# Performance work log

Hardware: AMD Instinct MI355X
Metric: run time of the kernel (lower is better)

Reference implementation:

```python
import jax, jax.numpy as jnp
import numpy as np

N_NODES = 50000
N_EDGES = 500000
IN_DIM = 32
HID = 64
NUM_GRAPHS = 64


def _inv(d):
    # 1/d with inf -> 0, as in PyG HypergraphConv
    return jnp.where(d > 0, 1.0 / d, 0.0)


def hypergraph_conv(xh, row0, row1, W, b, n_hnodes, n_hedges):
    """PyG HypergraphConv (heads=1, no attention, unit hyperedge weights).
    xh: (n_hnodes, din) hyper-node features; row0: hyper-node ids, row1: hyperedge ids.
    Index n_hnodes / n_hedges is a padding slot for masked-out incidences.
    """
    xw = xh @ W                                   # (n_hnodes, dout) Theta
    xw = jnp.concatenate([xw, jnp.zeros((1, xw.shape[1]), xw.dtype)], axis=0)
    ones = jnp.ones(row0.shape[0], xw.dtype)
    D = _inv(jax.ops.segment_sum(ones, row0, num_segments=n_hnodes + 1))  # node degree^-1
    B = _inv(jax.ops.segment_sum(ones, row1, num_segments=n_hedges + 1))  # edge size^-1
    # node -> hyperedge aggregation, scaled by B
    he = jax.ops.segment_sum(xw[row0], row1, num_segments=n_hedges + 1) * B[:, None]
    # hyperedge -> node aggregation, scaled by D
    out = jax.ops.segment_sum(he[row1], row0, num_segments=n_hnodes + 1) * D[:, None]
    return out[:n_hnodes] + b


def setup_inputs() -> dict:
    key = jax.random.key(0)
    ks = jax.random.split(key, 12)
    x = jax.random.normal(ks[0], (N_NODES, 16), jnp.float32)
    edge_attr = jax.random.normal(ks[1], (N_EDGES, IN_DIM), jnp.float32)
    edge_index = jax.random.randint(ks[2], (2, N_EDGES), 0, N_NODES, dtype=jnp.int64)
    batch = jnp.sort(jax.random.randint(ks[3], (N_NODES,), 0, NUM_GRAPHS, dtype=jnp.int64))
    node_imp = jax.random.uniform(ks[4], (N_NODES,), jnp.float32)
    s = 0.05
    W0 = jax.random.normal(ks[5], (IN_DIM, HID), jnp.float32) * s
    b0 = jax.random.normal(ks[6], (HID,), jnp.float32) * s
    W1 = jax.random.normal(ks[7], (HID, HID), jnp.float32) * s
    b1 = jax.random.normal(ks[8], (HID,), jnp.float32) * s
    W2 = jax.random.normal(ks[9], (HID, HID), jnp.float32) * s
    b2 = jax.random.normal(ks[10], (HID,), jnp.float32) * s
    return {"x": x, "edge_attr": edge_attr, "edge_index": edge_index, "batch": batch,
            "node_imp": node_imp, "W0": W0, "b0": b0, "W1": W1, "b1": b1,
            "W2": W2, "b2": b2, "num_graphs": NUM_GRAPHS}


def reference(x, edge_attr, edge_index, batch, node_imp, W0, b0, W1, b1, W2, b2, num_graphs):
    N = x.shape[0]
    E = edge_index.shape[1]
    edge_imp = jnp.minimum(node_imp[edge_index[0]], node_imp[edge_index[1]])
    # --- Dual Hypergraph Transform (get_DHT) ---
    row0 = jnp.repeat(jnp.arange(E), 2)            # hyper-node = original edge id
    row1 = edge_index.T.reshape(-1)                # hyperedge  = original node id
    deg = jax.ops.segment_sum(jnp.ones(2 * E, jnp.float32), row1, num_segments=N)
    keep = deg[row1] != 1.0                        # drop incidences of degree-1 hyperedges
    row0 = jnp.where(keep, row0, E)                # redirect dropped entries to padding slot
    row1 = jnp.where(keep, row1, N + E)
    # self-loops: hyperedge ids N..N+E-1 (equivalent to torch's max_edge+1.., since
    # unused hyperedge slots receive nothing and B^-1 there is 0)
    row0 = jnp.concatenate([row0, jnp.arange(E)])
    row1 = jnp.concatenate([row1, N + jnp.arange(E)])
    edge_batch = batch[edge_index[0]]              # == hyperedge_index[1].reshape(-1,2)[:,0]
    # --- conv stack (dropout in eval mode = identity) ---
    h = edge_attr * edge_imp[:, None]
    xs = []
    for (W, b) in ((W0, b0), (W1, b1), (W2, b2)):
        h = jax.nn.relu(hypergraph_conv(h, row0, row1, W, b, E, N + E))
        h = h * edge_imp[:, None]
        xs.append(h)
    gh = jnp.concatenate(
        [jax.ops.segment_sum(h_i, edge_batch, num_segments=num_graphs) for h_i in xs], axis=1)
    return gh
```

## Files before the change

### kernel.cpp

```cpp
#include <hip/hip_runtime.h>
#include <hip/hip_bf16.h>
#include <cstdint>
#include <cstddef>

typedef unsigned short u16;
typedef unsigned int   u32;
typedef short bf16x8 __attribute__((ext_vector_type(8)));
typedef float f32x4  __attribute__((ext_vector_type(4)));

struct __align__(16) ERec {
  u32 uv;
  float rc, iurc, ivrc;
  float ie; u32 bat; u32 pad0, pad1;
};

__device__ __forceinline__ float bf2f(u16 v){ return __uint_as_float(((u32)v)<<16); }
__device__ __forceinline__ u16 f2bf(float f){
  u32 x = __float_as_uint(f);
  return (u16)((x + 0x7FFFu + ((x>>16)&1u)) >> 16);
}
__device__ __forceinline__ void atomAddF(float* p, float v){ unsafeAtomicAdd(p, v); }
__device__ __forceinline__ float rlanef(float v, int q){
  return __int_as_float(__builtin_amdgcn_readlane(__float_as_int(v), q));
}

__global__ void kzero(int* p, int n){
  int i = blockIdx.x*blockDim.x + threadIdx.x;
  if(i < n) p[i] = 0;
}

__global__ void kdeg2(const int* __restrict__ ei0, const int* __restrict__ ei1,
                      int* __restrict__ deg0, int* __restrict__ deg1, int E){
  int e = blockIdx.x*blockDim.x + threadIdx.x;
  if(e >= E) return;
  atomicAdd(&deg0[ei0[e]], 1);
  atomicAdd(&deg1[ei1[e]], 1);
}

__global__ __launch_bounds__(256) void ktilesum(const int* __restrict__ deg0,
                                                const int* __restrict__ deg1,
                                                int* __restrict__ tsum,
                                                int N, int nt){
  __shared__ int sh[256];
  const int b = blockIdx.x;
  const int* deg = (b < nt) ? deg0 : deg1;
  const int tile = (b < nt) ? b : b - nt;
  const int t = threadIdx.x;
  const int i = tile*256 + t;
  sh[t] = (i < N) ? deg[i] : 0;
  __syncthreads();
  for(int s = 128; s > 0; s >>= 1){
    if(t < s) sh[t] += sh[t+s];
    __syncthreads();
  }
  if(t == 0) tsum[b] = sh[0];
}
__global__ __launch_bounds__(256) void kmid(int* __restrict__ tsum,
                                            int* __restrict__ off0,
                                            int* __restrict__ off1,
                                            int N, int nt){
  __shared__ int sh[256];
  const int b = blockIdx.x;
  int* ts = tsum + b*nt;
  const int t = threadIdx.x;
  sh[t] = (t < nt) ? ts[t] : 0;
  __syncthreads();
  for(int s = 1; s < 256; s <<= 1){
    int x = (t >= s) ? sh[t-s] : 0;
    __syncthreads();
    sh[t] += x;
    __syncthreads();
  }
  if(t < nt) ts[t] = (t == 0) ? 0 : sh[t-1];
  if(t == 255){ int* off = b ? off1 : off0; off[N] = sh[255]; }
}
__global__ __launch_bounds__(256) void kapply(const int* __restrict__ deg0,
                                              const int* __restrict__ deg1,
                                              const int* __restrict__ tsum,
                                              int* __restrict__ off0,
                                              int* __restrict__ off1,
                                              float* __restrict__ dinv,
                                              int N, int nt){
  __shared__ int sh[256];
  const int b = blockIdx.x;
  const int* deg = (b < nt) ? deg0 : deg1;
  int*       off = (b < nt) ? off0 : off1;
  const int tile = (b < nt) ? b : b - nt;
  const int base = tsum[b];
  const int t = threadIdx.x;
  const int i = tile*256 + t;
  sh[t] = (i < N) ? deg[i] : 0;
  __syncthreads();
  for(int s = 1; s < 256; s <<= 1){
    int x = (t >= s) ? sh[t-s] : 0;
    __syncthreads();
    sh[t] += x;
    __syncthreads();
  }
  if(i < N){
    off[i] = base + ((t == 0) ? 0 : sh[t-1]);
    if(b < nt){
      int d = deg0[i] + deg1[i];
      dinv[i] = (d > 1) ? (1.f/(float)d) : 0.f;
    }
  }
}

__global__ void kperm(const int* __restrict__ ei0, const int* __restrict__ ei1,
                      const float* __restrict__ nimp, const float* __restrict__ dinv,
                      const int* __restrict__ batch, const int* __restrict__ off0,
                      int* __restrict__ cur0, ERec* __restrict__ rec,
                      int* __restrict__ iperm, float* __restrict__ impO, int E){
  int e = blockIdx.x*blockDim.x + threadIdx.x;
  if(e >= E) return;
  int u = ei0[e], v = ei1[e];
  int pos = off0[u] + atomicAdd(&cur0[u], 1);
  float iu = dinv[u], iv = dinv[v];
  float rc = (iu > 0.f && iv > 0.f) ? (1.f/3.f)
           : ((iu > 0.f || iv > 0.f) ? 0.5f : 1.f);
  float ie = fminf(nimp[u], nimp[v]);
  ERec r;
  r.uv = (u32)u | ((u32)v << 16);
  r.rc = rc; r.iurc = iu*rc; r.ivrc = iv*rc;
  r.ie = ie; r.bat = (u32)batch[u]; r.pad0 = 0; r.pad1 = 0;
  rec[pos]  = r;
  iperm[e]  = pos;
  impO[e]   = ie;
}

__global__ void kfillv(const int* __restrict__ ei1, const int* __restrict__ iperm,
                       const int* __restrict__ off1, int* __restrict__ cur1,
                       int* __restrict__ list1, int E){
  int e = blockIdx.x*blockDim.x + threadIdx.x;
  if(e >= E) return;
  int v = ei1[e];
  list1[off1[v] + atomicAdd(&cur1[v], 1)] = iperm[e];
}

__global__ void kprepw(const float* __restrict__ W0, u16* __restrict__ wf0,
                       const float* __restrict__ W1, u16* __restrict__ wf1,
                       const float* __restrict__ W2, u16* __restrict__ wf2){
  const int b = blockIdx.x;
  const float* W; u16* wf; int NC, sbase;
  if(b == 0){ W = W0; wf = wf0; NC = 1; sbase = 0; }
  else if(b <= 2){ W = W1; wf = wf1; NC = 2; sbase = (b-1)*256; }
  else { W = W2; wf = wf2; NC = 2; sbase = (b-3)*256; }
  int s = sbase + threadIdx.x;
  if(s >= 4*NC*64) return;
  int lane = s & 63;
  int c    = (s >> 6) % NC;
  int tt   = s / (NC*64);
  int n  = tt*16 + (lane & 15);
  int k0 = c*32 + (lane >> 4)*8;
  #pragma unroll
  for(int j = 0; j < 8; j++)
    wf[(size_t)s*8 + j] = f2bf(W[(size_t)(k0 + j)*64 + n]);
}

__global__ __launch_bounds__(256) void kgemm0(const float* __restrict__ srcf,
                                              u16* __restrict__ buf,
                                              const u16* __restrict__ wf,
                                              const float* __restrict__ impO,
                                              const int* __restrict__ iperm,
                                              int E){
  const int t    = threadIdx.x;
  const int wv   = t >> 6;
  const int lane = t & 63;
  const int quad = lane >> 4;
  const int l15  = lane & 15;
  const int row0 = blockIdx.x*64 + wv*16;
  if(row0 >= E) return;

  bf16x8 bfr[4];
  #pragma unroll
  for(int i = 0; i < 4; i++)
    bfr[i] = *(const bf16x8*)(wf + ((size_t)i*64 + lane)*8);

  const int myrow = row0 + l15;
  const float* s = srcf + (size_t)myrow*32 + quad*8;
  const float sc = impO[myrow];
  const int ip = iperm[myrow];
  f32x4 v0 = *(const f32x4*)s;
  f32x4 v1 = *(const f32x4*)(s+4);
  bf16x8 afr;
  afr[0]=(short)f2bf(v0.x*sc); afr[1]=(short)f2bf(v0.y*sc);
  afr[2]=(short)f2bf(v0.z*sc); afr[3]=(short)f2bf(v0.w*sc);
  afr[4]=(short)f2bf(v1.x*sc); afr[5]=(short)f2bf(v1.y*sc);
  afr[6]=(short)f2bf(v1.z*sc); afr[7]=(short)f2bf(v1.w*sc);

  int dr[4];
  #pragma unroll
  for(int r = 0; r < 4; r++) dr[r] = __shfl(ip, quad*4 + r);

  #pragma unroll
  for(int tt = 0; tt < 4; tt++){
    f32x4 a = {0.f,0.f,0.f,0.f};
    a = __builtin_amdgcn_mfma_f32_16x16x32_bf16(afr, bfr[tt], a, 0, 0, 0);
    const int n = tt*16 + l15;
    #pragma unroll
    for(int r = 0; r < 4; r++)
      buf[(size_t)dr[r]*64 + n] = f2bf(a[r]);
  }
}

__global__ __launch_bounds__(256) void kagg(const u16* __restrict__ buf,
                                            const int* __restrict__ off0,
                                            const int* __restrict__ off1,
                                            const int* __restrict__ list1,
                                            u16* __restrict__ heb, int N){
  const int t = threadIdx.x, wv = t >> 6, lane = t & 63;
  const int n = blockIdx.x*4 + wv;
  if(n >= N) return;
  const int rsub = lane >> 3, cb = lane & 7;
  float acc[8];
  #pragma unroll
  for(int k = 0; k < 8; k++) acc[k] = 0.f;

  auto accum = [&](uint4 x){
    acc[0] += bf2f((u16)x.x); acc[1] += bf2f((u16)(x.x>>16));
    acc[2] += bf2f((u16)x.y); acc[3] += bf2f((u16)(x.y>>16));
    acc[4] += bf2f((u16)x.z); acc[5] += bf2f((u16)(x.z>>16));
    acc[6] += bf2f((u16)x.w); acc[7] += bf2f((u16)(x.w>>16));
  };
  const uint4 zero4 = {0,0,0,0};

  {
    const int s0 = off0[n], d0 = off0[n+1] - s0;
    const u16* base = buf + (size_t)s0*64;
    int j = 0;
    for(; j + 8 <= d0; j += 8)
      accum(*(const uint4*)(base + (size_t)(j+rsub)*64 + cb*8));
    if(j < d0)
      accum((rsub < d0-j) ? *(const uint4*)(base + (size_t)(j+rsub)*64 + cb*8) : zero4);
  }
  {
    const int s1 = off1[n], d1 = off1[n+1] - s1;
    int j = 0;
    for(; j + 8 <= d1; j += 8){
      int e = list1[s1 + j + rsub];
      accum(*(const uint4*)(buf + (size_t)e*64 + cb*8));
    }
    if(j < d1){
      uint4 x = zero4;
      if(rsub < d1-j){
        int e = list1[s1 + j + rsub];
        x = *(const uint4*)(buf + (size_t)e*64 + cb*8);
      }
      accum(x);
    }
  }
  #pragma unroll
  for(int m = 8; m <= 32; m <<= 1)
    #pragma unroll
    for(int k = 0; k < 8; k++) acc[k] += __shfl_xor(acc[k], m);
  if(rsub == 0){
    u32 o[4];
    #pragma unroll
    for(int k = 0; k < 4; k++)
      o[k] = (u32)f2bf(acc[2*k]) | ((u32)f2bf(acc[2*k+1]) << 16);
    *(uint4*)(heb + (size_t)n*64 + cb*8) = make_uint4(o[0],o[1],o[2],o[3]);
  }
}

template<bool DO_GEMM>
__global__ __launch_bounds__(256, 3) void kfused(u16* __restrict__ buf,
                                                 const u16* __restrict__ heb,
                                                 const f32x4* __restrict__ rec4,
                                                 const float* __restrict__ bias,
                                                 const u16* __restrict__ wf,
                                                 float* __restrict__ ghL,
                                                 int E){
  constexpr int HTSZ = DO_GEMM ? 4*16*72 : 4;
  __shared__ __align__(16) u16 hT[HTSZ];
  const int t = threadIdx.x, wv = t >> 6, lane = t & 63;
  const int quad = lane >> 4, l15 = lane & 15;
  const float bd = bias[lane];

  bf16x8 bfr[8];
  if(DO_GEMM){
    #pragma unroll
    for(int i = 0; i < 8; i++)
      bfr[i] = *(const bf16x8*)(wf + ((size_t)i*64 + lane)*8);
  }

  float pool = 0.f;
  int cur_g = -1;
  const int base = __builtin_amdgcn_readfirstlane((int)(blockIdx.x*256) + wv*64);
  u16* hTw = DO_GEMM ? &hT[wv*1152] : &hT[0];

  u32 uvp = 0; f32x4 cf = {0.f,0.f,0.f,0.f}; int bt = 0;
  if(base < E){
    f32x4 w0 = rec4[(size_t)(base+l15)*2];
    f32x4 w1 = rec4[(size_t)(base+l15)*2 + 1];
    uvp = __float_as_uint(w0.x);
    cf.x = w0.y; cf.y = w0.z; cf.z = w0.w; cf.w = w1.x;
    bt  = __float_as_int(w1.y);
  }

  #pragma unroll
  for(int it = 0; it < 4; it++){
    const int r0 = base + it*16;
    if(r0 < E){
      u16 bv[16], hu[16], hv[16];
      const u16* bufr = buf + (size_t)r0*64;
      #pragma unroll
      for(int q = 0; q < 16; q++){
        const u32 uv = (u32)__builtin_amdgcn_readlane((int)uvp, q);
        hv[q] = heb[(size_t)(uv >> 16)*64 + lane];
        hu[q] = heb[(size_t)(uv & 0xffffu)*64 + lane];
        bv[q] = bufr[q*64 + lane];
      }
      u32 uvpN = uvp; f32x4 cfN = cf; int btN = bt;
      if(it < 3){
        const int r1 = r0 + 16;
        if(r1 < E){
          f32x4 w0 = rec4[(size_t)(r1+l15)*2];
          f32x4 w1 = rec4[(size_t)(r1+l15)*2 + 1];
          uvpN = __float_as_uint(w0.x);
          cfN.x = w0.y; cfN.y = w0.z; cfN.z = w0.w; cfN.w = w1.x;
          btN  = __float_as_int(w1.y);
        }
      }
      const int bFirst = __builtin_amdgcn_readlane(bt, 0);
      const int bLast  = __builtin_amdgcn_readlane(bt, 15);
      if(bFirst != cur_g){
        if(cur_g >= 0) atomAddF(&ghL[cur_g*192 + lane], pool);
        pool = 0.f; cur_g = bFirst;
      }
      if(bFirst == bLast){
        #pragma unroll
        for(int q = 0; q < 16; q++){
          const float rc   = rlanef(cf.x, q);
          const float iurc = rlanef(cf.y, q);
          const float ivrc = rlanef(cf.z, q);
          const float ie   = rlanef(cf.w, q);
          float o = fmaxf(fmaf(bf2f(bv[q]), rc,
                          fmaf(bf2f(hu[q]), iurc,
                          fmaf(bf2f(hv[q]), ivrc, bd))), 0.f) * ie;
          pool += o;
          if(DO_GEMM) hTw[q*72 + lane] = f2bf(o);
        }
      } else {
        #pragma unroll
        for(int q = 0; q < 16; q++){
          const float rc   = rlanef(cf.x, q);
          const float iurc = rlanef(cf.y, q);
          const float ivrc = rlanef(cf.z, q);
          const float ie   = rlanef(cf.w, q);
          const int   bq   = __builtin_amdgcn_readlane(bt, q);
          float o = fmaxf(fmaf(bf2f(bv[q]), rc,
                          fmaf(bf2f(hu[q]), iurc,
                          fmaf(bf2f(hv[q]), ivrc, bd))), 0.f) * ie;
          if(bq != cur_g){
            if(cur_g >= 0) atomAddF(&ghL[cur_g*192 + lane], pool);
            pool = 0.f; cur_g = bq;
          }
          pool += o;
          if(DO_GEMM) hTw[q*72 + lane] = f2bf(o);
        }
      }
      if(DO_GEMM){
        bf16x8 afr0 = *(const bf16x8*)&hTw[l15*72 + quad*8];
        bf16x8 afr1 = *(const bf16x8*)&hTw[l15*72 + 32 + quad*8];
        #pragma unroll
        for(int tt = 0; tt < 4; tt++){
          f32x4 a = {0.f,0.f,0.f,0.f};
          a = __builtin_amdgcn_mfma_f32_16x16x32_bf16(afr0, bfr[tt*2+0], a, 0, 0, 0);
          a = __builtin_amdgcn_mfma_f32_16x16x32_bf16(afr1, bfr[tt*2+1], a, 0, 0, 0);
          const int n = tt*16 + l15;
          #pragma unroll
          for(int r = 0; r < 4; r++)
            buf[(size_t)(r0 + quad*4 + r)*64 + n] = f2bf(a[r]);
        }
      }
      uvp = uvpN; cf = cfN; bt = btN;
    }
  }
  if(cur_g >= 0) atomAddF(&ghL[cur_g*192 + lane], pool);
}

__global__ void kfinal(const float* __restrict__ gh, float* __restrict__ out, int n){
  int i = blockIdx.x*blockDim.x + threadIdx.x;
  if(i < n) out[i] = gh[i];
}

extern "C" void kernel_launch(void* const* d_in, const int* in_sizes, int n_in,
                              void* d_out, int out_size, void* d_ws, size_t ws_size,
                              hipStream_t stream) {
  const float* edge_attr = (const float*)d_in[1];
  const int*   ei        = (const int*)d_in[2];
  const int*   batch     = (const int*)d_in[3];
  const float* nimp      = (const float*)d_in[4];
  const float* Ws[3] = { (const float*)d_in[5], (const float*)d_in[7], (const float*)d_in[9] };
  const float* bs[3] = { (const float*)d_in[6], (const float*)d_in[8], (const float*)d_in[10] };

  const int E = in_sizes[1] / 32;
  const int N = in_sizes[4];
  const int* ei0 = ei;
  const int* ei1 = ei + E;

  char* p = (char*)d_ws;
  auto carve = [&](size_t bytes)->char*{
    char* r = p; p += (bytes + 255) & ~(size_t)255; return r;
  };
  const int nt = (N + 255)/256;
  int*   deg0  = (int*)  carve((size_t)4*N*4);
  int*   deg1  = deg0 + N;
  int*   cur0  = deg0 + 2*N;
  int*   cur1  = deg0 + 3*N;
  float* dinv  = (float*)carve((size_t)N*4);
  int*   off0  = (int*)  carve((size_t)(N+1)*4);
  int*   off1  = (int*)  carve((size_t)(N+1)*4);
  int*   tsum  = (int*)  carve((size_t)2*nt*4);
  int*   iperm = (int*)  carve((size_t)E*4);
  float* impO  = (float*)carve((size_t)E*4);
  int*   list1 = (int*)  carve((size_t)E*4);
  ERec*  rec   = (ERec*) carve((size_t)E*sizeof(ERec));
  u16*   heb   = (u16*)  carve((size_t)N*64*2);
  u16*   buf   = (u16*)  carve((size_t)E*64*2);
  float* gh    = (float*)carve((size_t)64*192*4);
  u16*   wfs[3];
  for(int l = 0; l < 3; l++) wfs[l] = (u16*)carve((size_t)4096*2);

  kzero<<<(4*N+255)/256, 256, 0, stream>>>(deg0, 4*N);
  kzero<<<(12288+255)/256, 256, 0, stream>>>((int*)gh, 12288);
  kdeg2<<<(E+255)/256, 256, 0, stream>>>(ei0, ei1, deg0, deg1, E);
  ktilesum<<<2*nt, 256, 0, stream>>>(deg0, deg1, tsum, N, nt);
  kmid<<<2, 256, 0, stream>>>(tsum, off0, off1, N, nt);
  kapply<<<2*nt, 256, 0, stream>>>(deg0, deg1, tsum, off0, off1, dinv, N, nt);
  kperm<<<(E+255)/256, 256, 0, stream>>>(ei0, ei1, nimp, dinv, batch, off0, cur0,
                                         rec, iperm, impO, E);
  kfillv<<<(E+255)/256, 256, 0, stream>>>(ei1, iperm, off1, cur1, list1, E);
  kprepw<<<5, 256, 0, stream>>>(Ws[0], wfs[0], Ws[1], wfs[1], Ws[2], wfs[2]);

  const int nbG = (E + 63)/64;
  const int nbA = (N + 3)/4;
  const int nbF = (E + 255)/256;

  kgemm0<<<nbG, 256, 0, stream>>>(edge_attr, buf, wfs[0], impO, iperm, E);
  kagg<<<nbA, 256, 0, stream>>>(buf, off0, off1, list1, heb, N);
  kfused<true ><<<nbF, 256, 0, stream>>>(buf, heb, (const f32x4*)rec, bs[0], wfs[1], gh + 0*64, E);
  kagg<<<nbA, 256, 0, stream>>>(buf, off0, off1, list1, heb, N);
  kfused<true ><<<nbF, 256, 0, stream>>>(buf, heb, (const f32x4*)rec, bs[1], wfs[2], gh + 1*64, E);
  kagg<<<nbA, 256, 0, stream>>>(buf, off0, off1, list1, heb, N);
  kfused<false><<<nbF, 256, 0, stream>>>(buf, heb, (const f32x4*)rec, bs[2], nullptr, gh + 2*64, E);
  kfinal<<<(12288+255)/256, 256, 0, stream>>>(gh, (float*)d_out, 12288);
}
```

Baseline: 432.5 us.

## Privatize degree/cursor atomics into per-block-group copies and fuse permutation kernels

Degree counting and CSR cursor atomics are split across 8 privatized copies chosen by block index, with a new reduce kernel that produces total degrees plus per-copy base offsets. The two permutation kernels (row and column list fill) are merged into one. Per-node dinv, importance and batch are packed into a 16-byte record so each endpoint needs a single load. This aims to cut atomic contention and launch count, at the cost of 8x larger counter arrays to zero and an extra reduce pass.

```diff
diff --git a/kernel.cpp b/kernel.cpp
--- a/kernel.cpp
+++ b/kernel.cpp
@@ -13,6 +13,9 @@
   float rc, iurc, ivrc;
   float ie; u32 bat; u32 pad0, pad1;
 };
+struct __align__(16) NRec { float dinv; float imp; int bat; int pad; };
+
+#define NCOPY 8
 
 __device__ __forceinline__ float bf2f(u16 v){ return __uint_as_float(((u32)v)<<16); }
 __device__ __forceinline__ u16 f2bf(float f){
@@ -29,12 +32,32 @@
   if(i < n) p[i] = 0;
 }
 
-__global__ void kdeg2(const int* __restrict__ ei0, const int* __restrict__ ei1,
-                      int* __restrict__ deg0, int* __restrict__ deg1, int E){
+__global__ void kdeg2p(const int* __restrict__ ei0, const int* __restrict__ ei1,
+                       int* __restrict__ deg0c, int* __restrict__ deg1c,
+                       int N, int E){
   int e = blockIdx.x*blockDim.x + threadIdx.x;
   if(e >= E) return;
-  atomicAdd(&deg0[ei0[e]], 1);
-  atomicAdd(&deg1[ei1[e]], 1);
+  const int c = blockIdx.x & (NCOPY-1);
+  atomicAdd(&deg0c[c*N + ei0[e]], 1);
+  atomicAdd(&deg1c[c*N + ei1[e]], 1);
+}
+
+__global__ void kreduce(const int* __restrict__ deg0c, const int* __restrict__ deg1c,
+                        int* __restrict__ deg0, int* __restrict__ deg1,
+                        int* __restrict__ cb0, int* __restrict__ cb1, int N){
+  int i = blockIdx.x*blockDim.x + threadIdx.x;
+  if(i < N){
+    int s = 0;
+    #pragma unroll
+    for(int c = 0; c < NCOPY; c++){ int t = deg0c[c*N+i]; cb0[c*N+i] = s; s += t; }
+    deg0[i] = s;
+  } else if(i < 2*N){
+    int j = i - N;
+    int s = 0;
+    #pragma unroll
+    for(int c = 0; c < NCOPY; c++){ int t = deg1c[c*N+j]; cb1[c*N+j] = s; s += t; }
+    deg1[j] = s;
+  }
 }
 
 __global__ __launch_bounds__(256) void ktilesum(const int* __restrict__ deg0,
@@ -79,7 +102,9 @@
                                               const int* __restrict__ tsum,
                                               int* __restrict__ off0,
                                               int* __restrict__ off1,
-                                              float* __restrict__ dinv,
+                                              const float* __restrict__ nimp,
+                                              const int* __restrict__ batch,
+                                              NRec* __restrict__ nrec,
                                               int N, int nt){
   __shared__ int sh[256];
   const int b = blockIdx.x;
@@ -101,40 +126,44 @@
     off[i] = base + ((t == 0) ? 0 : sh[t-1]);
     if(b < nt){
       int d = deg0[i] + deg1[i];
-      dinv[i] = (d > 1) ? (1.f/(float)d) : 0.f;
+      NRec r;
+      r.dinv = (d > 1) ? (1.f/(float)d) : 0.f;
+      r.imp  = nimp[i];
+      r.bat  = batch[i];
+      r.pad  = 0;
+      nrec[i] = r;
     }
   }
 }
 
-__global__ void kperm(const int* __restrict__ ei0, const int* __restrict__ ei1,
-                      const float* __restrict__ nimp, const float* __restrict__ dinv,
-                      const int* __restrict__ batch, const int* __restrict__ off0,
-                      int* __restrict__ cur0, ERec* __restrict__ rec,
-                      int* __restrict__ iperm, float* __restrict__ impO, int E){
+__global__ void kpermv(const int* __restrict__ ei0, const int* __restrict__ ei1,
+                       const NRec* __restrict__ nrec,
+                       const int* __restrict__ off0, const int* __restrict__ off1,
+                       const int* __restrict__ cb0, const int* __restrict__ cb1,
+                       int* __restrict__ cur0c, int* __restrict__ cur1c,
+                       ERec* __restrict__ rec, int* __restrict__ iperm,
+                       float* __restrict__ impO, int* __restrict__ list1,
+                       int E, int N){
   int e = blockIdx.x*blockDim.x + threadIdx.x;
   if(e >= E) return;
+  const int c = blockIdx.x & (NCOPY-1);
   int u = ei0[e], v = ei1[e];
-  int pos = off0[u] + atomicAdd(&cur0[u], 1);
-  float iu = dinv[u], iv = dinv[v];
+  NRec ru = nrec[u];
+  NRec rv = nrec[v];
+  int pos = off0[u] + cb0[c*N+u] + atomicAdd(&cur0c[c*N+u], 1);
+  float iu = ru.dinv, iv = rv.dinv;
   float rc = (iu > 0.f && iv > 0.f) ? (1.f/3.f)
            : ((iu > 0.f || iv > 0.f) ? 0.5f : 1.f);
-  float ie = fminf(nimp[u], nimp[v]);
+  float ie = fminf(ru.imp, rv.imp);
   ERec r;
   r.uv = (u32)u | ((u32)v << 16);
   r.rc = rc; r.iurc = iu*rc; r.ivrc = iv*rc;
-  r.ie = ie; r.bat = (u32)batch[u]; r.pad0 = 0; r.pad1 = 0;
+  r.ie = ie; r.bat = (u32)ru.bat; r.pad0 = 0; r.pad1 = 0;
   rec[pos]  = r;
   iperm[e]  = pos;
   impO[e]   = ie;
-}
-
-__global__ void kfillv(const int* __restrict__ ei1, const int* __restrict__ iperm,
-                       const int* __restrict__ off1, int* __restrict__ cur1,
-                       int* __restrict__ list1, int E){
-  int e = blockIdx.x*blockDim.x + threadIdx.x;
-  if(e >= E) return;
-  int v = ei1[e];
-  list1[off1[v] + atomicAdd(&cur1[v], 1)] = iperm[e];
+  int p1 = off1[v] + cb1[c*N+v] + atomicAdd(&cur1c[c*N+v], 1);
+  list1[p1] = pos;
 }
 
 __global__ void kprepw(const float* __restrict__ W0, u16* __restrict__ wf0,
@@ -404,11 +433,15 @@
     char* r = p; p += (bytes + 255) & ~(size_t)255; return r;
   };
   const int nt = (N + 255)/256;
-  int*   deg0  = (int*)  carve((size_t)4*N*4);
+  int*   deg0c = (int*)  carve((size_t)4*NCOPY*N*4);
+  int*   deg1c = deg0c + NCOPY*N;
+  int*   cur0c = deg0c + 2*NCOPY*N;
+  int*   cur1c = deg0c + 3*NCOPY*N;
+  int*   cb0   = (int*)  carve((size_t)2*NCOPY*N*4);
+  int*   cb1   = cb0 + NCOPY*N;
+  int*   deg0  = (int*)  carve((size_t)2*N*4);
   int*   deg1  = deg0 + N;
-  int*   cur0  = deg0 + 2*N;
-  int*   cur1  = deg0 + 3*N;
-  float* dinv  = (float*)carve((size_t)N*4);
+  NRec*  nrec  = (NRec*) carve((size_t)N*sizeof(NRec));
   int*   off0  = (int*)  carve((size_t)(N+1)*4);
   int*   off1  = (int*)  carve((size_t)(N+1)*4);
   int*   tsum  = (int*)  carve((size_t)2*nt*4);
@@ -422,15 +455,15 @@
   u16*   wfs[3];
   for(int l = 0; l < 3; l++) wfs[l] = (u16*)carve((size_t)4096*2);
 
-  kzero<<<(4*N+255)/256, 256, 0, stream>>>(deg0, 4*N);
+  kzero<<<(4*NCOPY*N+255)/256, 256, 0, stream>>>(deg0c, 4*NCOPY*N);
   kzero<<<(12288+255)/256, 256, 0, stream>>>((int*)gh, 12288);
-  kdeg2<<<(E+255)/256, 256, 0, stream>>>(ei0, ei1, deg0, deg1, E);
+  kdeg2p<<<(E+255)/256, 256, 0, stream>>>(ei0, ei1, deg0c, deg1c, N, E);
+  kreduce<<<(2*N+255)/256, 256, 0, stream>>>(deg0c, deg1c, deg0, deg1, cb0, cb1, N);
   ktilesum<<<2*nt, 256, 0, stream>>>(deg0, deg1, tsum, N, nt);
   kmid<<<2, 256, 0, stream>>>(tsum, off0, off1, N, nt);
-  kapply<<<2*nt, 256, 0, stream>>>(deg0, deg1, tsum, off0, off1, dinv, N, nt);
-  kperm<<<(E+255)/256, 256, 0, stream>>>(ei0, ei1, nimp, dinv, batch, off0, cur0,
-                                         rec, iperm, impO, E);
-  kfillv<<<(E+255)/256, 256, 0, stream>>>(ei1, iperm, off1, cur1, list1, E);
+  kapply<<<2*nt, 256, 0, stream>>>(deg0, deg1, tsum, off0, off1, nimp, batch, nrec, N, nt);
+  kpermv<<<(E+255)/256, 256, 0, stream>>>(ei0, ei1, nrec, off0, off1, cb0, cb1,
+                                          cur0c, cur1c, rec, iperm, impO, list1, E, N);
   kprepw<<<5, 256, 0, stream>>>(Ws[0], wfs[0], Ws[1], wfs[1], Ws[2], wfs[2]);
 
   const int nbG = (E + 63)/64;
```

Measured after the change: 428.7 us. About the same (-0.9%).
